# Kernel tuning notes

Measured on AMD Instinct MI355X. Metric: run time of the kernel, lower is better.

Reference implementation:

```python
import jax, jax.numpy as jnp
import numpy as np

N = 50000      # nodes
E = 800000     # edges
F_IN = 500     # input features
H1 = 300       # lin output
H2 = 100       # conv1 output
C = 16         # num classes


def setup_inputs() -> dict:
    key = jax.random.key(0)
    ks = jax.random.split(key, 8)
    x = jax.random.normal(ks[0], (N, F_IN), dtype=jnp.float32)
    edge_index = jax.random.randint(ks[1], (2, E), 0, N, dtype=jnp.int64)
    s = 0.05
    lin_W = jax.random.normal(ks[2], (F_IN, H1), dtype=jnp.float32) * s
    lin_b = jnp.zeros((H1,), dtype=jnp.float32)
    W1 = jax.random.normal(ks[3], (H1, H2), dtype=jnp.float32) * s
    b1 = jnp.zeros((H2,), dtype=jnp.float32)
    W2 = jax.random.normal(ks[4], (H2, C), dtype=jnp.float32) * s
    b2 = jnp.zeros((C,), dtype=jnp.float32)
    return {"x": x, "lin_W": lin_W, "lin_b": lin_b, "W1": W1, "b1": b1,
            "W2": W2, "b2": b2, "edge_index": edge_index}


def gcn_layer(x, W, b, src, dst):
    # project first (PyG GCNConv), then normalized gather-scatter aggregation
    h = x @ W                                   # [N, d_out]
    loops = jnp.arange(N, dtype=src.dtype)      # add self-loops
    s = jnp.concatenate([src, loops])           # [E+N]
    d = jnp.concatenate([dst, loops])
    deg = jax.ops.segment_sum(jnp.ones_like(d, dtype=h.dtype), d, num_segments=N)
    dinv = jax.lax.rsqrt(jnp.maximum(deg, 1.0))  # deg >= 1 due to self-loops
    norm = dinv[s] * dinv[d]                     # [E+N]
    out = jax.ops.segment_sum(h[s] * norm[:, None], d, num_segments=N)
    return out + b


def reference(x, lin_W, lin_b, W1, b1, W2, b2, edge_index):
    src, dst = edge_index[0], edge_index[1]
    h = jax.nn.relu(x @ lin_W + lin_b)          # Linear(500->300) + relu
    h = jax.nn.relu(gcn_layer(h, W1, b1, src, dst))  # GCNConv(300->100) + relu
    # dropout is identity at inference (training=False)
    h = gcn_layer(h, W2, b2, src, dst)          # GCNConv(100->16)
    return jax.nn.log_softmax(h, axis=1)
```

## Files before the change

kernel.cpp:

```cpp
#include <hip/hip_runtime.h>
#include <hip/hip_bf16.h>

#define NN 50000
#define EE 800000
#define FIN 500
#define H1D 300
#define H2D 100
#define CC 16

__device__ __forceinline__ float ldf(const void* p, size_t i, int isbf16) {
    return isbf16 ? __bfloat162float(((const __hip_bfloat16*)p)[i])
                  : ((const float*)p)[i];
}
__device__ __forceinline__ int ld_src(const int* ei, int e, int is64) {
    return is64 ? ei[2 * (size_t)e] : ei[e];
}
__device__ __forceinline__ int ld_dst(const int* ei, int e, int is64) {
    return is64 ? ei[2 * ((size_t)EE + e)] : ei[(size_t)EE + e];
}

__device__ __forceinline__ void split2(float f, unsigned short& h, unsigned short& l) {
    __bf16 hb = (__bf16)f;
    float fh = (float)hb;
    __bf16 lb = (__bf16)(f - fh);
    h = __builtin_bit_cast(unsigned short, hb);
    l = __builtin_bit_cast(unsigned short, lb);
}

__device__ __forceinline__ float2 bf2f2(unsigned int v) {
    float lo = __builtin_bit_cast(float, v << 16);
    float hi = __builtin_bit_cast(float, v & 0xffff0000u);
    return make_float2(lo, hi);
}

typedef __bf16 bf16x8 __attribute__((ext_vector_type(8)));
typedef float f32x4 __attribute__((ext_vector_type(4)));

__global__ __launch_bounds__(256) void k_init(const unsigned short* __restrict__ xw,
                                              const unsigned int* __restrict__ ew,
                                              int* __restrict__ flags,
                                              int* __restrict__ cnt,
                                              int* __restrict__ total) {
    if (blockIdx.x == 0) {
        __shared__ int c_sane, c_zero;
        if (threadIdx.x == 0) { c_sane = 0; c_zero = 0; }
        __syncthreads();
        int t = threadIdx.x;
        int sane = 0, zer = 0;
        for (int j = 0; j < 4; j++) {
            unsigned short w = xw[t * 4 + j];
            int ex = (w >> 7) & 0xFF;
            if (w == 0 || (ex >= 100 && ex <= 150)) sane++;
            if (ew[2 * (t * 4 + j) + 1] == 0u) zer++;
        }
        atomicAdd(&c_sane, sane);
        atomicAdd(&c_zero, zer);
        __syncthreads();
        if (threadIdx.x == 0) {
            flags[0] = (c_sane > 820) ? 1 : 0;
            flags[1] = (c_zero > 512) ? 1 : 0;
            total[0] = 0;
        }
    } else {
        int i = (blockIdx.x - 1) * 256 + threadIdx.x;
        if (i < NN) cnt[i] = 0;
    }
}

__global__ void k_hist(const int* __restrict__ ei, int* __restrict__ cnt,
                       const int* __restrict__ flags) {
    int e = blockIdx.x * blockDim.x + threadIdx.x;
    int is64 = flags[1];
    if (e < EE) {
        int d = ld_dst(ei, e, is64);
        if ((unsigned)d < NN) atomicAdd(&cnt[d], 1);
    }
}

__global__ __launch_bounds__(256) void k_scan_mb(int* __restrict__ cnt,
                                                 int* __restrict__ row_ptr,
                                                 float* __restrict__ dinv,
                                                 int* __restrict__ total) {
    int t = threadIdx.x;
    int i = blockIdx.x * 256 + t;
    int c = (i < NN) ? cnt[i] : 0;
    __shared__ int s[256];
    s[t] = c;
    __syncthreads();
    for (int off = 1; off < 256; off <<= 1) {
        int v = (t >= off) ? s[t - off] : 0;
        __syncthreads();
        s[t] += v;
        __syncthreads();
    }
    int incl = s[t];
    __shared__ int base;
    if (t == 255) base = atomicAdd(total, s[255]);
    __syncthreads();
    if (i < NN) {
        row_ptr[i] = base + incl - c;
        dinv[i] = rsqrtf((float)c + 1.0f);
        cnt[i] = 0;
    }
}

__global__ void k_scatter(const int* __restrict__ ei, const int* __restrict__ row_ptr,
                          int* __restrict__ fill, int* __restrict__ csr_src,
                          const int* __restrict__ flags) {
    int e = blockIdx.x * blockDim.x + threadIdx.x;
    int is64 = flags[1];
    if (e < EE) {
        int s = ld_src(ei, e, is64);
        int d = ld_dst(ei, e, is64);
        if ((unsigned)d < NN) {
            int pos = row_ptr[d] + atomicAdd(&fill[d], 1);
            csr_src[pos] = s;
        }
    }
}

template <bool A_DYN, bool RELU, bool SCALE, bool OUTBF>
__global__ __launch_bounds__(256) void k_gemm(const void* __restrict__ A,
                                              const void* __restrict__ B,
                                              const void* __restrict__ bias,
                                              const float* __restrict__ dinv,
                                              void* __restrict__ C,
                                              int M, int K, int Nn,
                                              const int* __restrict__ flags) {
    if (!flags[0]) return;
    __shared__ float As[16][68];
    __shared__ float Bs[16][68];
    const int bf = flags[0];
    const int tid = threadIdx.x;
    const int m0 = blockIdx.x * 64, n0 = blockIdx.y * 64;
    const int tx = tid & 15;
    const int ty = tid >> 4;
    float acc[4][4] = {};

    for (int kc = 0; kc < K; kc += 16) {
#pragma unroll
        for (int j = 0; j < 4; j++) {
            int idx = tid + j * 256;
            int kk = idx & 15, mm = idx >> 4;
            int gm = m0 + mm, gk = kc + kk;
            float v = 0.0f;
            if (gm < M && gk < K) {
                size_t o = (size_t)gm * K + gk;
                v = A_DYN ? ldf(A, o, bf) : ((const float*)A)[o];
            }
            As[kk][mm] = v;
        }
#pragma unroll
        for (int j = 0; j < 4; j++) {
            int idx = tid + j * 256;
            int nn = idx & 63, kk = idx >> 6;
            int gk = kc + kk, gn = n0 + nn;
            Bs[kk][nn] = (gk < K && gn < Nn) ? ldf(B, (size_t)gk * Nn + gn, bf) : 0.0f;
        }
        __syncthreads();
#pragma unroll
        for (int kk = 0; kk < 16; kk++) {
            float4 a4 = *(const float4*)&As[kk][ty * 4];
            float4 b4 = *(const float4*)&Bs[kk][tx * 4];
            float av[4] = {a4.x, a4.y, a4.z, a4.w};
            float bv[4] = {b4.x, b4.y, b4.z, b4.w};
#pragma unroll
            for (int i = 0; i < 4; i++)
#pragma unroll
                for (int j = 0; j < 4; j++) acc[i][j] += av[i] * bv[j];
        }
        __syncthreads();
    }

#pragma unroll
    for (int i = 0; i < 4; i++) {
        int m = m0 + ty * 4 + i;
        if (m >= M) continue;
        float sc = SCALE ? dinv[m] : 1.0f;
#pragma unroll
        for (int j = 0; j < 4; j++) {
            int n = n0 + tx * 4 + j;
            if (n >= Nn) continue;
            float v = acc[i][j];
            if (bias) v += ldf(bias, n, bf);
            if (SCALE) v *= sc;
            if (RELU) v = fmaxf(v, 0.0f);
            if (OUTBF) ((__hip_bfloat16*)C)[(size_t)m * Nn + n] = __float2bfloat16(v);
            else       ((float*)C)[(size_t)m * Nn + n] = v;
        }
    }
}

__global__ __launch_bounds__(256) void k_prep_both(const float* __restrict__ linW,
                                                   const float* __restrict__ W1,
                                                   unsigned short* __restrict__ Bt1,
                                                   unsigned short* __restrict__ Bt2,
                                                   const int* __restrict__ flags) {
    if (flags[0]) return;
    int idx = blockIdx.x * 256 + threadIdx.x;
    const int n1 = 384 * 512;
    const int n2 = 128 * 320;
    if (idx < n1) {
        int n = idx >> 9, k = idx & 511;
        float v = (n < H1D && k < FIN) ? linW[(size_t)k * H1D + n] : 0.0f;
        unsigned short h, l;
        split2(v, h, l);
        Bt1[(size_t)n * 1024 + k] = h;
        Bt1[(size_t)n * 1024 + 512 + k] = l;
    } else if (idx < n1 + n2) {
        idx -= n1;
        int n = idx / 320, k = idx - n * 320;
        float v = (n < H2D && k < H1D) ? W1[(size_t)k * H2D + n] : 0.0f;
        unsigned short h, l;
        split2(v, h, l);
        Bt2[(size_t)n * 640 + k] = h;
        Bt2[(size_t)n * 640 + 320 + k] = l;
    }
}

template <int BM, int WN, bool RELU, bool SCALE, bool HAS_BIAS, bool OUTBF>
__global__ __launch_bounds__(256) void k_gemm_mfma_split(const float* __restrict__ A,
                                                         const unsigned short* __restrict__ Bt,
                                                         const float* __restrict__ bias,
                                                         const float* __restrict__ dinv,
                                                         void* __restrict__ C,
                                                         int M, int K, int Kp, int Nn,
                                                         const int* __restrict__ flags) {
    if (flags[0]) return;
    constexpr int WM = 4 / WN;
    constexpr int FM = BM / WM / 16;
    constexpr int FN = 128 / WN / 16;
    constexpr int NA = BM / 32;
    __shared__ unsigned short As_hi[BM * 32], As_lo[BM * 32];
    __shared__ unsigned short Bs_hi[4096], Bs_lo[4096];
    const int tid = threadIdx.x;
    const int nbx = gridDim.x;
    const int Wt = nbx * gridDim.y;
    const int li = blockIdx.x + nbx * blockIdx.y;
    const int q8 = Wt >> 3, r8 = Wt & 7;
    const int xk = li & 7, xj = li >> 3;
    const int wid = (xk < r8 ? xk * (q8 + 1) : r8 * (q8 + 1) + (xk - r8) * q8) + xj;
    const int n0 = (wid % nbx) * 128;
    const int m0 = (wid / nbx) * BM;
    const int w = tid >> 6, l = tid & 63;
    const int wm = (w / WN) * (BM / WM);
    const int wn = (w % WN) * (128 / WN);
    const int lr = l & 15, ls = l >> 4;
    f32x4 acc[FM][FN] = {};

    float4 stA[NA];
    uint4  stB0, stB1, stB2, stB3;

#define LOAD_TILE(kc_)                                                              \
    {                                                                               \
        int kc = (kc_);                                                             \
        _Pragma("unroll")                                                           \
        for (int j = 0; j < NA; j++) {                                              \
            int c = tid + j * 256;                                                  \
            int r = c >> 3, q = c & 7;                                              \
            int gm = m0 + r, gk = kc + q * 4;                                       \
            stA[j] = (gm < M && gk < K) ? *(const float4*)(A + (size_t)gm * K + gk) \
                                        : make_float4(0.f, 0.f, 0.f, 0.f);          \
        }                                                                           \
        {                                                                           \
            int c, r, q, gn;                                                        \
            c = tid;       r = c >> 2; q = c & 3; gn = n0 + r;                      \
            stB0 = *(const uint4*)(Bt + (size_t)gn * (2 * Kp) + kc + q * 8);        \
            c = tid + 256; r = c >> 2; q = c & 3; gn = n0 + r;                      \
            stB1 = *(const uint4*)(Bt + (size_t)gn * (2 * Kp) + kc + q * 8);        \
            c = tid;       r = c >> 2; q = c & 3; gn = n0 + r;                      \
            stB2 = *(const uint4*)(Bt + (size_t)gn * (2 * Kp) + Kp + kc + q * 8);   \
            c = tid + 256; r = c >> 2; q = c & 3; gn = n0 + r;                      \
            stB3 = *(const uint4*)(Bt + (size_t)gn * (2 * Kp) + Kp + kc + q * 8);   \
        }                                                                           \
    }

#define WRITE_TILE()                                                                \
    {                                                                               \
        _Pragma("unroll")                                                           \
        for (int j = 0; j < NA; j++) {                                              \
            int c = tid + j * 256;                                                  \
            int r = c >> 3, q = c & 7;                                              \
            unsigned short h0,h1,h2,h3,l0,l1,l2,l3;                                 \
            split2(stA[j].x, h0, l0); split2(stA[j].y, h1, l1);                     \
            split2(stA[j].z, h2, l2); split2(stA[j].w, h3, l3);                     \
            int waddr = r * 64 + (((q >> 1) ^ ((r >> 1) & 3)) << 4) + ((q & 1) << 3); \
            *(ushort4*)((char*)As_hi + waddr) = make_ushort4(h0, h1, h2, h3);       \
            *(ushort4*)((char*)As_lo + waddr) = make_ushort4(l0, l1, l2, l3);       \
        }                                                                           \
        {                                                                           \
            int c, r, q, waddr;                                                     \
            c = tid;       r = c >> 2; q = c & 3; waddr = r * 64 + ((q ^ ((r >> 1) & 3)) << 4); \
            *(uint4*)((char*)Bs_hi + waddr) = stB0;                                 \
            c = tid + 256; r = c >> 2; q = c & 3; waddr = r * 64 + ((q ^ ((r >> 1) & 3)) << 4); \
            *(uint4*)((char*)Bs_hi + waddr) = stB1;                                 \
            c = tid;       r = c >> 2; q = c & 3; waddr = r * 64 + ((q ^ ((r >> 1) & 3)) << 4); \
            *(uint4*)((char*)Bs_lo + waddr) = stB2;                                 \
            c = tid + 256; r = c >> 2; q = c & 3; waddr = r * 64 + ((q ^ ((r >> 1) & 3)) << 4); \
            *(uint4*)((char*)Bs_lo + waddr) = stB3;                                 \
        }                                                                           \
    }

    const int nsteps = (K + 31) / 32;
    LOAD_TILE(0);
    for (int kt = 0; kt < nsteps; kt++) {
        WRITE_TILE();
        __syncthreads();
        if (kt + 1 < nsteps) LOAD_TILE((kt + 1) * 32);
        bf16x8 ah[FM], al[FM], bh[FN], bl[FN];
#pragma unroll
        for (int fm = 0; fm < FM; fm++) {
            int rr = wm + fm * 16 + lr;
            int addr = rr * 64 + ((ls ^ ((rr >> 1) & 3)) << 4);
            ah[fm] = *(const bf16x8*)((const char*)As_hi + addr);
            al[fm] = *(const bf16x8*)((const char*)As_lo + addr);
        }
#pragma unroll
        for (int fn = 0; fn < FN; fn++) {
            int cc2 = wn + fn * 16 + lr;
            int addr = cc2 * 64 + ((ls ^ ((cc2 >> 1) & 3)) << 4);
            bh[fn] = *(const bf16x8*)((const char*)Bs_hi + addr);
            bl[fn] = *(const bf16x8*)((const char*)Bs_lo + addr);
        }
#pragma unroll
        for (int fm = 0; fm < FM; fm++)
#pragma unroll
            for (int fn = 0; fn < FN; fn++) {
                acc[fm][fn] = __builtin_amdgcn_mfma_f32_16x16x32_bf16(ah[fm], bh[fn], acc[fm][fn], 0, 0, 0);
                acc[fm][fn] = __builtin_amdgcn_mfma_f32_16x16x32_bf16(ah[fm], bl[fn], acc[fm][fn], 0, 0, 0);
                acc[fm][fn] = __builtin_amdgcn_mfma_f32_16x16x32_bf16(al[fm], bh[fn], acc[fm][fn], 0, 0, 0);
            }
        __syncthreads();
    }
#undef LOAD_TILE
#undef WRITE_TILE

#pragma unroll
    for (int fm = 0; fm < FM; fm++) {
#pragma unroll
        for (int j = 0; j < 4; j++) {
            int m = m0 + wm + fm * 16 + ls * 4 + j;
            if (m >= M) continue;
            float sc = SCALE ? dinv[m] : 1.0f;
#pragma unroll
            for (int fn = 0; fn < FN; fn++) {
                int n = n0 + wn + fn * 16 + lr;
                if (n >= Nn) continue;
                float v = acc[fm][fn][j];
                if (HAS_BIAS) v += bias[n];
                if (SCALE) v *= sc;
                if (RELU) v = fmaxf(v, 0.0f);
                if (OUTBF) ((__hip_bfloat16*)C)[(size_t)m * Nn + n] = __float2bfloat16(v);
                else       ((float*)C)[(size_t)m * Nn + n] = v;
            }
        }
    }
}

__global__ __launch_bounds__(256) void k_agg1_fused(const unsigned short* __restrict__ h1p_bf,
                                                    const int* __restrict__ row_ptr,
                                                    const int* __restrict__ deg,
                                                    const int* __restrict__ csr_src,
                                                    const float* __restrict__ dinv,
                                                    const void* __restrict__ b1,
                                                    const void* __restrict__ W2,
                                                    float* __restrict__ h2p,
                                                    const int* __restrict__ flags) {
    __shared__ float W2s[16][105];
    __shared__ float b1s[H2D];
    __shared__ float Hrow[4][H2D];
    const int bf = flags[0];
    const int tid = threadIdx.x;
    for (int i = tid; i < H2D * CC; i += 256) {
        int k = i >> 4, n = i & 15;
        W2s[n][k] = ldf(W2, i, bf);
    }
    for (int i = tid; i < H2D; i += 256) b1s[i] = ldf(b1, i, bf);
    __syncthreads();

    const int w = tid >> 6, lane = tid & 63;
    const int q = lane >> 4, n16 = lane & 15;
    const unsigned int* rows = (const unsigned int*)h1p_bf;
    for (int node = blockIdx.x * 4 + w; node < NN; node += gridDim.x * 4) {
        float di = dinv[node];
        if (lane < 50) {
            float2 s = bf2f2(rows[(size_t)node * 50 + lane]);
            float a0x = s.x, a0y = s.y;
            float a1x = 0.f, a1y = 0.f, a2x = 0.f, a2y = 0.f, a3x = 0.f, a3y = 0.f;
            int lo = row_ptr[node], hi = lo + deg[node];
            int e = lo;
            for (; e + 3 < hi; e += 4) {
                int s0 = csr_src[e], s1 = csr_src[e + 1], s2 = csr_src[e + 2], s3 = csr_src[e + 3];
                float2 v0 = bf2f2(rows[(size_t)s0 * 50 + lane]);
                float2 v1 = bf2f2(rows[(size_t)s1 * 50 + lane]);
                float2 v2 = bf2f2(rows[(size_t)s2 * 50 + lane]);
                float2 v3 = bf2f2(rows[(size_t)s3 * 50 + lane]);
                a0x += v0.x; a0y += v0.y;
                a1x += v1.x; a1y += v1.y;
                a2x += v2.x; a2y += v2.y;
                a3x += v3.x; a3y += v3.y;
            }
            for (; e < hi; e++) {
                float2 v = bf2f2(rows[(size_t)csr_src[e] * 50 + lane]);
                a0x += v.x; a0y += v.y;
            }
            float sx = (a0x + a1x) + (a2x + a3x);
            float sy = (a0y + a1y) + (a2y + a3y);
            int f = lane * 2;
            Hrow[w][f]     = fmaxf(sx * di + b1s[f], 0.0f);
            Hrow[w][f + 1] = fmaxf(sy * di + b1s[f + 1], 0.0f);
        }
        __builtin_amdgcn_sched_barrier(0);
        float acc2 = 0.0f;
#pragma unroll
        for (int j = 0; j < 25; j++) {
            int k = q * 25 + j;
            acc2 += Hrow[w][k] * W2s[n16][k];
        }
        acc2 += __shfl_xor(acc2, 16);
        acc2 += __shfl_xor(acc2, 32);
        if (lane < 16) h2p[(size_t)node * CC + n16] = acc2 * di;
        __builtin_amdgcn_sched_barrier(0);
    }
}

__global__ __launch_bounds__(256) void k_agg2(const float* __restrict__ h2p,
                                              const int* __restrict__ row_ptr,
                                              const int* __restrict__ deg,
                                              const int* __restrict__ csr_src,
                                              const float* __restrict__ dinv,
                                              const void* __restrict__ b2,
                                              void* __restrict__ out,
                                              const int* __restrict__ flags) {
    int tid = threadIdx.x;
    int n = tid & 15;
    int g = tid >> 4;
    int node = blockIdx.x * 16 + g;
    if (node >= NN) return;
    const int bf = flags[0];
    float a0 = h2p[(size_t)node * CC + n];
    float a1 = 0.f, a2 = 0.f, a3 = 0.f;
    int lo = row_ptr[node], hi = lo + deg[node];
    int e = lo;
    for (; e + 3 < hi; e += 4) {
        int s0 = csr_src[e], s1 = csr_src[e + 1], s2 = csr_src[e + 2], s3 = csr_src[e + 3];
        a0 += h2p[(size_t)s0 * CC + n];
        a1 += h2p[(size_t)s1 * CC + n];
        a2 += h2p[(size_t)s2 * CC + n];
        a3 += h2p[(size_t)s3 * CC + n];
    }
    for (; e < hi; e++) a0 += h2p[(size_t)csr_src[e] * CC + n];
    float acc = (a0 + a1) + (a2 + a3);
    float logit = acc * dinv[node] + ldf(b2, n, bf);
    float m = logit;
#pragma unroll
    for (int off = 1; off < 16; off <<= 1) m = fmaxf(m, __shfl_xor(m, off, 16));
    float ex = __expf(logit - m);
    float ssum = ex;
#pragma unroll
    for (int off = 1; off < 16; off <<= 1) ssum += __shfl_xor(ssum, off, 16);
    float r = logit - m - __logf(ssum);
    size_t oidx = (size_t)node * CC + n;
    if (bf) ((__hip_bfloat16*)out)[oidx] = __float2bfloat16(r);
    else    ((float*)out)[oidx] = r;
}

extern "C" void kernel_launch(void* const* d_in, const int* in_sizes, int n_in,
                              void* d_out, int out_size, void* d_ws, size_t ws_size,
                              hipStream_t stream) {
    const void* x     = d_in[0];
    const void* lin_W = d_in[1];
    const void* lin_b = d_in[2];
    const void* W1    = d_in[3];
    const void* b1    = d_in[4];
    const void* W2    = d_in[5];
    const void* b2    = d_in[6];
    const int*  ei    = (const int*)d_in[7];

    char* ws = (char*)d_ws;
    size_t off = 0;
    auto alloc = [&](size_t bytes) {
        off = (off + 255) & ~(size_t)255;
        void* p = ws + off;
        off += bytes;
        return p;
    };
    int*   flags   = (int*)alloc(2 * 4);
    int*   total   = (int*)alloc(4);
    int*   cnt     = (int*)alloc((size_t)NN * 4);
    int*   row_ptr = (int*)alloc((size_t)NN * 4);
    int*   csr_src = (int*)alloc((size_t)EE * 4);
    float* dinv    = (float*)alloc((size_t)NN * 4);
    float* H1      = (float*)alloc((size_t)NN * H1D * 4);
    unsigned short* H1p = (unsigned short*)alloc((size_t)NN * H2D * 2);
    float* h2p     = (float*)alloc((size_t)NN * CC * 4);
    unsigned short* Bt1 = (unsigned short*)alloc((size_t)384 * 1024 * 2);
    unsigned short* Bt2 = (unsigned short*)alloc((size_t)128 * 640 * 2);

    const int gN = (NN + 255) / 256;
    const int gE = (EE + 255) / 256;

    const bool surely_fp32 = (in_sizes != nullptr) && (in_sizes[0] >= 90000000);

    k_init<<<gN + 1, 256, 0, stream>>>((const unsigned short*)x, (const unsigned int*)ei,
                                       flags, cnt, total);
    k_hist<<<gE, 256, 0, stream>>>(ei, cnt, flags);
    k_scan_mb<<<gN, 256, 0, stream>>>(cnt, row_ptr, dinv, total);
    k_scatter<<<gE, 256, 0, stream>>>(ei, row_ptr, cnt, csr_src, flags);

    k_prep_both<<<(384 * 512 + 128 * 320 + 255) / 256, 256, 0, stream>>>(
        (const float*)lin_W, (const float*)W1, Bt1, Bt2, flags);

    k_gemm_mfma_split<64, 4, true, false, true, false>
        <<<dim3(3, (NN + 63) / 64), 256, 0, stream>>>(
            (const float*)x, Bt1, (const float*)lin_b, nullptr, H1, NN, FIN, 512, H1D, flags);
    if (!surely_fp32) {
        dim3 grid((NN + 63) / 64, (H1D + 63) / 64);
        k_gemm<true, true, false, false><<<grid, 256, 0, stream>>>(
            x, lin_W, lin_b, nullptr, H1, NN, FIN, H1D, flags);
    }

    k_gemm_mfma_split<64, 4, false, true, false, true>
        <<<dim3(1, (NN + 63) / 64), 256, 0, stream>>>(
            H1, Bt2, nullptr, dinv, H1p, NN, H1D, 320, H2D, flags);
    if (!surely_fp32) {
        dim3 grid((NN + 63) / 64, (H2D + 63) / 64);
        k_gemm<false, false, true, true><<<grid, 256, 0, stream>>>(
            H1, W1, nullptr, dinv, H1p, NN, H1D, H2D, flags);
    }

    k_agg1_fused<<<6144, 256, 0, stream>>>(H1p, row_ptr, cnt, csr_src, dinv, b1, W2, h2p, flags);
    k_agg2<<<(NN + 15) / 16, 256, 0, stream>>>(h2p, row_ptr, cnt, csr_src, dinv, b2, d_out, flags);
}
```

Baseline: 420.6 us.

## Store H1 as padded bf16 and use single-bf16-A GEMM for layer two

The first GEMM now writes its ReLU output as bf16 with a 320-column padded stride, and it is launched in four row chunks. A new second-layer GEMM reads that bf16 activation directly and does two MFMAs per tile (A times B-hi and B-lo) instead of the three-term split-precision scheme. Weight preparation moves into the init kernel to save a launch. The intent is to halve H1 memory traffic and cut MFMA work, at the cost of rounding the intermediate activation to bf16. The fallback fp32 path still writes H1 as float, which may be inconsistent with the new bf16 reader.

```diff
diff --git a/kernel.cpp b/kernel.cpp
--- a/kernel.cpp
+++ b/kernel.cpp
@@ -7,6 +7,10 @@
 #define H1D 300
 #define H2D 100
 #define CC 16
+#define GNB 196
+#define PREP_N1 196608
+#define PREP_N2 40960
+#define PREP_BLOCKS 928
 
 __device__ __forceinline__ float ldf(const void* p, size_t i, int isbf16) {
     return isbf16 ? __bfloat162float(((const __hip_bfloat16*)p)[i])
@@ -36,12 +40,37 @@
 typedef __bf16 bf16x8 __attribute__((ext_vector_type(8)));
 typedef float f32x4 __attribute__((ext_vector_type(4)));
 
+__device__ __forceinline__ void prep_body(int idx, const float* linW, const float* W1,
+                                          unsigned short* Bt1, unsigned short* Bt2) {
+    if (idx < PREP_N1) {
+        int n = idx >> 9, k = idx & 511;
+        float v = (n < H1D && k < FIN) ? linW[(size_t)k * H1D + n] : 0.0f;
+        unsigned short h, l;
+        split2(v, h, l);
+        Bt1[(size_t)n * 1024 + k] = h;
+        Bt1[(size_t)n * 1024 + 512 + k] = l;
+    } else if (idx < PREP_N1 + PREP_N2) {
+        idx -= PREP_N1;
+        int n = idx / 320, k = idx - n * 320;
+        float v = (n < H2D && k < H1D) ? W1[(size_t)k * H2D + n] : 0.0f;
+        unsigned short h, l;
+        split2(v, h, l);
+        Bt2[(size_t)n * 640 + k] = h;
+        Bt2[(size_t)n * 640 + 320 + k] = l;
+    }
+}
+
 __global__ __launch_bounds__(256) void k_init(const unsigned short* __restrict__ xw,
                                               const unsigned int* __restrict__ ew,
                                               int* __restrict__ flags,
                                               int* __restrict__ cnt,
-                                              int* __restrict__ total) {
-    if (blockIdx.x == 0) {
+                                              int* __restrict__ total,
+                                              const float* __restrict__ linW,
+                                              const float* __restrict__ W1,
+                                              unsigned short* __restrict__ Bt1,
+                                              unsigned short* __restrict__ Bt2) {
+    int b = blockIdx.x;
+    if (b == 0) {
         __shared__ int c_sane, c_zero;
         if (threadIdx.x == 0) { c_sane = 0; c_zero = 0; }
         __syncthreads();
@@ -61,10 +90,21 @@
             flags[1] = (c_zero > 512) ? 1 : 0;
             total[0] = 0;
         }
+    } else if (b <= GNB) {
+        int i = (b - 1) * 256 + threadIdx.x;
+        if (i < NN) cnt[i] = 0;
     } else {
-        int i = (blockIdx.x - 1) * 256 + threadIdx.x;
-        if (i < NN) cnt[i] = 0;
-    }
+        prep_body((b - GNB - 1) * 256 + threadIdx.x, linW, W1, Bt1, Bt2);
+    }
+}
+
+__global__ __launch_bounds__(256) void k_prep_both(const float* __restrict__ linW,
+                                                   const float* __restrict__ W1,
+                                                   unsigned short* __restrict__ Bt1,
+                                                   unsigned short* __restrict__ Bt2,
+                                                   const int* __restrict__ flags) {
+    if (flags[0]) return;
+    prep_body(blockIdx.x * 256 + threadIdx.x, linW, W1, Bt1, Bt2);
 }
 
 __global__ void k_hist(const int* __restrict__ ei, int* __restrict__ cnt,
@@ -191,40 +231,13 @@
     }
 }
 
-__global__ __launch_bounds__(256) void k_prep_both(const float* __restrict__ linW,
-                                                   const float* __restrict__ W1,
-                                                   unsigned short* __restrict__ Bt1,
-                                                   unsigned short* __restrict__ Bt2,
-                                                   const int* __restrict__ flags) {
-    if (flags[0]) return;
-    int idx = blockIdx.x * 256 + threadIdx.x;
-    const int n1 = 384 * 512;
-    const int n2 = 128 * 320;
-    if (idx < n1) {
-        int n = idx >> 9, k = idx & 511;
-        float v = (n < H1D && k < FIN) ? linW[(size_t)k * H1D + n] : 0.0f;
-        unsigned short h, l;
-        split2(v, h, l);
-        Bt1[(size_t)n * 1024 + k] = h;
-        Bt1[(size_t)n * 1024 + 512 + k] = l;
-    } else if (idx < n1 + n2) {
-        idx -= n1;
-        int n = idx / 320, k = idx - n * 320;
-        float v = (n < H2D && k < H1D) ? W1[(size_t)k * H2D + n] : 0.0f;
-        unsigned short h, l;
-        split2(v, h, l);
-        Bt2[(size_t)n * 640 + k] = h;
-        Bt2[(size_t)n * 640 + 320 + k] = l;
-    }
-}
-
 template <int BM, int WN, bool RELU, bool SCALE, bool HAS_BIAS, bool OUTBF>
 __global__ __launch_bounds__(256) void k_gemm_mfma_split(const float* __restrict__ A,
                                                          const unsigned short* __restrict__ Bt,
                                                          const float* __restrict__ bias,
                                                          const float* __restrict__ dinv,
                                                          void* __restrict__ C,
-                                                         int M, int K, int Kp, int Nn,
+                                                         int M, int K, int Kp, int Nn, int NnS,
                                                          const int* __restrict__ flags) {
     if (flags[0]) return;
     constexpr int WM = 4 / WN;
@@ -345,13 +358,138 @@
 #pragma unroll
             for (int fn = 0; fn < FN; fn++) {
                 int n = n0 + wn + fn * 16 + lr;
-                if (n >= Nn) continue;
-                float v = acc[fm][fn][j];
-                if (HAS_BIAS) v += bias[n];
-                if (SCALE) v *= sc;
-                if (RELU) v = fmaxf(v, 0.0f);
-                if (OUTBF) ((__hip_bfloat16*)C)[(size_t)m * Nn + n] = __float2bfloat16(v);
-                else       ((float*)C)[(size_t)m * Nn + n] = v;
+                if (OUTBF) {
+                    if (n >= NnS) continue;
+                    float v = 0.0f;
+                    if (n < Nn) {
+                        v = acc[fm][fn][j];
+                        if (HAS_BIAS) v += bias[n];
+                        if (SCALE) v *= sc;
+                        if (RELU) v = fmaxf(v, 0.0f);
+                    }
+                    ((__hip_bfloat16*)C)[(size_t)m * NnS + n] = __float2bfloat16(v);
+                } else {
+                    if (n >= Nn) continue;
+                    float v = acc[fm][fn][j];
+                    if (HAS_BIAS) v += bias[n];
+                    if (SCALE) v *= sc;
+                    if (RELU) v = fmaxf(v, 0.0f);
+                    ((float*)C)[(size_t)m * Nn + n] = v;
+                }
+            }
+        }
+    }
+}
+
+__global__ __launch_bounds__(256) void k_gemm2_bf16a(const unsigned short* __restrict__ A,
+                                                     const unsigned short* __restrict__ Bt,
+                                                     const float* __restrict__ dinv,
+                                                     unsigned short* __restrict__ C,
+                                                     int M, const int* __restrict__ flags) {
+    if (flags[0]) return;
+    constexpr int Kp = 320;
+    __shared__ unsigned short As[64 * 32];
+    __shared__ unsigned short Bs_hi[4096], Bs_lo[4096];
+    const int tid = threadIdx.x;
+    const int Wt = gridDim.x;
+    const int li = blockIdx.x;
+    const int q8 = Wt >> 3, r8 = Wt & 7;
+    const int xk = li & 7, xj = li >> 3;
+    const int wid = (xk < r8 ? xk * (q8 + 1) : r8 * (q8 + 1) + (xk - r8) * q8) + xj;
+    const int m0 = wid * 64;
+    const int w = tid >> 6, l = tid & 63;
+    const int wn = w * 32;
+    const int lr = l & 15, ls = l >> 4;
+    f32x4 acc[4][2] = {};
+
+    uint4 stA, stB0, stB1, stB2, stB3;
+
+#define LOAD_T2(kc_)                                                                \
+    {                                                                               \
+        int kc = (kc_);                                                             \
+        {                                                                           \
+            int r = tid >> 2, q = tid & 3;                                          \
+            int gm = m0 + r;                                                        \
+            stA = (gm < M) ? *(const uint4*)(A + (size_t)gm * Kp + kc + q * 8)      \
+                           : make_uint4(0u, 0u, 0u, 0u);                            \
+        }                                                                           \
+        {                                                                           \
+            int c, r, q, gn;                                                        \
+            c = tid;       r = c >> 2; q = c & 3; gn = r;                           \
+            stB0 = *(const uint4*)(Bt + (size_t)gn * (2 * Kp) + kc + q * 8);        \
+            c = tid + 256; r = c >> 2; q = c & 3; gn = r;                           \
+            stB1 = *(const uint4*)(Bt + (size_t)gn * (2 * Kp) + kc + q * 8);        \
+            c = tid;       r = c >> 2; q = c & 3; gn = r;                           \
+            stB2 = *(const uint4*)(Bt + (size_t)gn * (2 * Kp) + Kp + kc + q * 8);   \
+            c = tid + 256; r = c >> 2; q = c & 3; gn = r;                           \
+            stB3 = *(const uint4*)(Bt + (size_t)gn * (2 * Kp) + Kp + kc + q * 8);   \
+        }                                                                           \
+    }
+
+#define WRITE_T2()                                                                  \
+    {                                                                               \
+        {                                                                           \
+            int r = tid >> 2, q = tid & 3;                                          \
+            int waddr = r * 64 + ((q ^ ((r >> 1) & 3)) << 4);                       \
+            *(uint4*)((char*)As + waddr) = stA;                                     \
+        }                                                                           \
+        {                                                                           \
+            int c, r, q, waddr;                                                     \
+            c = tid;       r = c >> 2; q = c & 3; waddr = r * 64 + ((q ^ ((r >> 1) & 3)) << 4); \
+            *(uint4*)((char*)Bs_hi + waddr) = stB0;                                 \
+            c = tid + 256; r = c >> 2; q = c & 3; waddr = r * 64 + ((q ^ ((r >> 1) & 3)) << 4); \
+            *(uint4*)((char*)Bs_hi + waddr) = stB1;                                 \
+            c = tid;       r = c >> 2; q = c & 3; waddr = r * 64 + ((q ^ ((r >> 1) & 3)) << 4); \
+            *(uint4*)((char*)Bs_lo + waddr) = stB2;                                 \
+            c = tid + 256; r = c >> 2; q = c & 3; waddr = r * 64 + ((q ^ ((r >> 1) & 3)) << 4); \
+            *(uint4*)((char*)Bs_lo + waddr) = stB3;                                 \
+        }                                                                           \
+    }
+
+    const int nsteps = Kp / 32;
+    LOAD_T2(0);
+    for (int kt = 0; kt < nsteps; kt++) {
+        WRITE_T2();
+        __syncthreads();
+        if (kt + 1 < nsteps) LOAD_T2((kt + 1) * 32);
+        bf16x8 ah[4], bh[2], bl[2];
+#pragma unroll
+        for (int fm = 0; fm < 4; fm++) {
+            int rr = fm * 16 + lr;
+            int addr = rr * 64 + ((ls ^ ((rr >> 1) & 3)) << 4);
+            ah[fm] = *(const bf16x8*)((const char*)As + addr);
+        }
+#pragma unroll
+        for (int fn = 0; fn < 2; fn++) {
+            int cc2 = wn + fn * 16 + lr;
+            int addr = cc2 * 64 + ((ls ^ ((cc2 >> 1) & 3)) << 4);
+            bh[fn] = *(const bf16x8*)((const char*)Bs_hi + addr);
+            bl[fn] = *(const bf16x8*)((const char*)Bs_lo + addr);
+        }
+#pragma unroll
+        for (int fm = 0; fm < 4; fm++)
+#pragma unroll
+            for (int fn = 0; fn < 2; fn++) {
+                acc[fm][fn] = __builtin_amdgcn_mfma_f32_16x16x32_bf16(ah[fm], bh[fn], acc[fm][fn], 0, 0, 0);
+                acc[fm][fn] = __builtin_amdgcn_mfma_f32_16x16x32_bf16(ah[fm], bl[fn], acc[fm][fn], 0, 0, 0);
+            }
+        __syncthreads();
+    }
+#undef LOAD_T2
+#undef WRITE_T2
+
+#pragma unroll
+    for (int fm = 0; fm < 4; fm++) {
+#pragma unroll
+        for (int j = 0; j < 4; j++) {
+            int m = m0 + fm * 16 + ls * 4 + j;
+            if (m >= M) continue;
+            float sc = dinv[m];
+#pragma unroll
+            for (int fn = 0; fn < 2; fn++) {
+                int n = wn + fn * 16 + lr;
+                if (n >= H2D) continue;
+                ((__hip_bfloat16*)C)[(size_t)m * H2D + n] = __float2bfloat16(acc[fm][fn][j] * sc);
             }
         }
     }
@@ -491,38 +629,47 @@
     int*   row_ptr = (int*)alloc((size_t)NN * 4);
     int*   csr_src = (int*)alloc((size_t)EE * 4);
     float* dinv    = (float*)alloc((size_t)NN * 4);
-    float* H1      = (float*)alloc((size_t)NN * H1D * 4);
+    char*  H1      = (char*)alloc((size_t)NN * H1D * 4);
     unsigned short* H1p = (unsigned short*)alloc((size_t)NN * H2D * 2);
     float* h2p     = (float*)alloc((size_t)NN * CC * 4);
     unsigned short* Bt1 = (unsigned short*)alloc((size_t)384 * 1024 * 2);
     unsigned short* Bt2 = (unsigned short*)alloc((size_t)128 * 640 * 2);
 
-    const int gN = (NN + 255) / 256;
     const int gE = (EE + 255) / 256;
 
     const bool surely_fp32 = (in_sizes != nullptr) && (in_sizes[0] >= 90000000);
 
-    k_init<<<gN + 1, 256, 0, stream>>>((const unsigned short*)x, (const unsigned int*)ei,
-                                       flags, cnt, total);
+    k_init<<<surely_fp32 ? (GNB + 1 + PREP_BLOCKS) : (GNB + 1), 256, 0, stream>>>(
+        (const unsigned short*)x, (const unsigned int*)ei, flags, cnt, total,
+        (const float*)lin_W, (const float*)W1, Bt1, Bt2);
+    if (!surely_fp32)
+        k_prep_both<<<PREP_BLOCKS, 256, 0, stream>>>(
+            (const float*)lin_W, (const float*)W1, Bt1, Bt2, flags);
+
     k_hist<<<gE, 256, 0, stream>>>(ei, cnt, flags);
-    k_scan_mb<<<gN, 256, 0, stream>>>(cnt, row_ptr, dinv, total);
+    k_scan_mb<<<GNB, 256, 0, stream>>>(cnt, row_ptr, dinv, total);
     k_scatter<<<gE, 256, 0, stream>>>(ei, row_ptr, cnt, csr_src, flags);
 
-    k_prep_both<<<(384 * 512 + 128 * 320 + 255) / 256, 256, 0, stream>>>(
-        (const float*)lin_W, (const float*)W1, Bt1, Bt2, flags);
-
-    k_gemm_mfma_split<64, 4, true, false, true, false>
-        <<<dim3(3, (NN + 63) / 64), 256, 0, stream>>>(
-            (const float*)x, Bt1, (const float*)lin_b, nullptr, H1, NN, FIN, 512, H1D, flags);
+    {
+        const int moff[5] = {0, 12544, 25088, 37632, 50000};
+        for (int qi = 0; qi < 4; qi++) {
+            int Mq = moff[qi + 1] - moff[qi];
+            int nb = (Mq + 63) / 64;
+            k_gemm_mfma_split<64, 4, true, false, true, true>
+                <<<dim3(3, nb), 256, 0, stream>>>(
+                    (const float*)x + (size_t)moff[qi] * FIN, Bt1, (const float*)lin_b,
+                    nullptr, (unsigned short*)H1 + (size_t)moff[qi] * 320,
+                    Mq, FIN, 512, H1D, 320, flags);
+        }
+    }
     if (!surely_fp32) {
         dim3 grid((NN + 63) / 64, (H1D + 63) / 64);
         k_gemm<true, true, false, false><<<grid, 256, 0, stream>>>(
             x, lin_W, lin_b, nullptr, H1, NN, FIN, H1D, flags);
     }
 
-    k_gemm_mfma_split<64, 4, false, true, false, true>
-        <<<dim3(1, (NN + 63) / 64), 256, 0, stream>>>(
-            H1, Bt2, nullptr, dinv, H1p, NN, H1D, 320, H2D, flags);
+    k_gemm2_bf16a<<<(NN + 63) / 64, 256, 0, stream>>>(
+        (const unsigned short*)H1, Bt2, dinv, H1p, NN, flags);
     if (!surely_fp32) {
         dim3 grid((NN + 63) / 64, (H2D + 63) / 64);
         k_gemm<false, false, true, true><<<grid, 256, 0, stream>>>(
```

Result: slower. 453.0 us (+7.7%).
